# Kernel optimization log

Measured on AMD Instinct MI355X. Metric: run time of the kernel, lower is better.

## Reference

```python
import jax, jax.numpy as jnp
import numpy as np

N_NODES = 50000
N_EDGES = 500000
D_IN, D_HID = 128, 256


def _add_self_loops(edge_index, n):
    loop = jnp.arange(n, dtype=edge_index.dtype)
    src = jnp.concatenate([edge_index[0], loop])
    dst = jnp.concatenate([edge_index[1], loop])
    return src, dst


def _gcn_layer(x, W, b, src, dst, dinv_sqrt, n):
    # x: [N, d_in] -> h: [N, d_out]
    h = x @ W
    # symmetric normalization D^{-1/2} (A+I) D^{-1/2}
    norm = dinv_sqrt[src] * dinv_sqrt[dst]          # [E+N]
    msg = h[src] * norm[:, None]                    # gather + scale
    agg = jax.ops.segment_sum(msg, dst, num_segments=n)  # scatter-add
    return agg + b


def setup_inputs() -> dict:
    key = jax.random.key(0)
    ks = jax.random.split(key, 8)
    x = jax.random.normal(ks[0], (N_NODES, D_IN), dtype=jnp.float32)
    edge_index = jax.random.randint(ks[1], (2, N_EDGES), 0, N_NODES, dtype=jnp.int64 if jax.config.read('jax_enable_x64') else jnp.int32)
    s = lambda fan_in: 1.0 / np.sqrt(fan_in)
    W1 = jax.random.uniform(ks[2], (D_IN, D_HID), jnp.float32, -s(D_IN), s(D_IN))
    b1 = jnp.zeros((D_HID,), jnp.float32)
    W2 = jax.random.uniform(ks[3], (D_HID, D_HID), jnp.float32, -s(D_HID), s(D_HID))
    b2 = jnp.zeros((D_HID,), jnp.float32)
    W3 = jax.random.uniform(ks[4], (D_HID, D_HID), jnp.float32, -s(D_HID), s(D_HID))
    b3 = jnp.zeros((D_HID,), jnp.float32)
    return {"x": x, "edge_index": edge_index, "W1": W1, "b1": b1,
            "W2": W2, "b2": b2, "W3": W3, "b3": b3}


def reference(x, edge_index, W1, b1, W2, b2, W3, b3):
    n = x.shape[0]
    src, dst = _add_self_loops(edge_index, n)
    # degree includes self loops (edge weight 1), as in torch_geometric GCNConv
    deg = jax.ops.segment_sum(jnp.ones_like(dst, dtype=x.dtype), dst, num_segments=n)
    dinv_sqrt = jnp.where(deg > 0, jax.lax.rsqrt(jnp.maximum(deg, 1e-12)), 0.0)
    h = jax.nn.relu(_gcn_layer(x, W1, b1, src, dst, dinv_sqrt, n))
    h = jax.nn.relu(_gcn_layer(h, W2, b2, src, dst, dinv_sqrt, n))
    h = _gcn_layer(h, W3, b3, src, dst, dinv_sqrt, n)
    return h
```

## Files before the change

### kernel.cpp

```cpp
#include <hip/hip_runtime.h>

#define NNODES 50000
#define NEDGES 500000
#define DIN 128
#define DHID 256
#define MPAD 50048
#define NI4 12500
#define NSB 49

typedef unsigned short u16;
typedef __attribute__((ext_vector_type(8))) _Float16 half8;
typedef __attribute__((ext_vector_type(4))) float f32x4;

__device__ __forceinline__ u16 f2h(float f) {
  union { _Float16 h; u16 u; } v; v.h = (_Float16)f; return v.u;
}
__device__ __forceinline__ float h2f(unsigned int u) {
  union { _Float16 h; u16 u; } v; v.u = (u16)u; return (float)v.h;
}

#define GLDS16(g, l) __builtin_amdgcn_global_load_lds( \
    (const __attribute__((address_space(1))) void*)(g), \
    (__attribute__((address_space(3))) void*)(l), 16, 0, 0)

__global__ void k_zero_i32(int* __restrict__ p, int n) {
  int i = blockIdx.x * blockDim.x + threadIdx.x;
  if (i < n) p[i] = 0;
}

__global__ void k_hist(const int* __restrict__ dst, int* __restrict__ deg, int e) {
  int i = blockIdx.x * blockDim.x + threadIdx.x;
  if (i < e) atomicAdd(&deg[dst[i]], 1);
}

__global__ __launch_bounds__(256) void k_blocksum(const int* __restrict__ deg,
                                                  int* __restrict__ partials) {
  __shared__ int red[256];
  int tid = threadIdx.x;
  int t4 = blockIdx.x * 256 + tid;
  int sum = 0;
  if (t4 < NI4) {
    int4 v = ((const int4*)deg)[t4];
    sum = v.x + v.y + v.z + v.w;
  }
  red[tid] = sum;
  __syncthreads();
  for (int off = 128; off > 0; off >>= 1) {
    if (tid < off) red[tid] += red[tid + off];
    __syncthreads();
  }
  if (tid == 0) partials[blockIdx.x] = red[0];
}

__global__ __launch_bounds__(256) void k_scan2(int* __restrict__ deg,
                                               const int* __restrict__ partials,
                                               int* __restrict__ row_ptr,
                                               float* __restrict__ dinv) {
  __shared__ int sdata[256];
  __shared__ int sprefix;
  int tid = threadIdx.x, bid = blockIdx.x;
  int t4 = bid * 256 + tid;
  int4 v = make_int4(0, 0, 0, 0);
  if (t4 < NI4) v = ((const int4*)deg)[t4];
  int tsum = v.x + v.y + v.z + v.w;
  sdata[tid] = tsum;
  if (tid == 0) {
    int pre = 0;
    for (int b = 0; b < bid; ++b) pre += partials[b];
    sprefix = pre;
  }
  __syncthreads();
  for (int off = 1; off < 256; off <<= 1) {
    int val = (tid >= off) ? sdata[tid - off] : 0;
    __syncthreads();
    sdata[tid] += val;
    __syncthreads();
  }
  if (t4 < NI4) {
    int run = sdata[tid] - tsum + sprefix;
    int base = t4 * 4;
    float4 dv;
    dv.x = rsqrtf((float)v.x + 1.0f);
    dv.y = rsqrtf((float)v.y + 1.0f);
    dv.z = rsqrtf((float)v.z + 1.0f);
    dv.w = rsqrtf((float)v.w + 1.0f);
    *(float4*)(dinv + base) = dv;
    row_ptr[base + 0] = run; run += v.x;
    row_ptr[base + 1] = run; run += v.y;
    row_ptr[base + 2] = run; run += v.z;
    row_ptr[base + 3] = run; run += v.w;
    if (base + 4 == NNODES) row_ptr[NNODES] = run;
    ((int4*)deg)[t4] = make_int4(0, 0, 0, 0);
  }
}

__global__ void k_fill(const int* __restrict__ src, const int* __restrict__ dst,
                       const float* __restrict__ dinv, const int* __restrict__ row_ptr,
                       int* __restrict__ cursor, int* __restrict__ csr_src,
                       float* __restrict__ csr_nrm, int e) {
  int i = blockIdx.x * blockDim.x + threadIdx.x;
  if (i < e) {
    int d = dst[i], s = src[i];
    int pos = row_ptr[d] + atomicAdd(&cursor[d], 1);
    csr_src[pos] = s;
    csr_nrm[pos] = dinv[s] * dinv[d];
  }
}

__global__ void k_x2f16(const float* __restrict__ x, u16* __restrict__ xh, int total4) {
  int i = blockIdx.x * blockDim.x + threadIdx.x;
  if (i >= total4) return;
  float4 v = ((const float4*)x)[i];
  ushort4 o;
  o.x = f2h(v.x); o.y = f2h(v.y); o.z = f2h(v.z); o.w = f2h(v.w);
  ((ushort4*)xh)[i] = o;
}

__global__ void k_splitW3(const float* __restrict__ W1f, u16* __restrict__ P1,
                          const float* __restrict__ W2f, u16* __restrict__ P2,
                          const float* __restrict__ W3f, u16* __restrict__ P3) {
  int i = blockIdx.x * blockDim.x + threadIdx.x;
  const int s1 = DIN * 256, s2 = s1 + DHID * 256, s3 = s2 + DHID * 256;
  if (i >= s3) return;
  const float* W; u16* P; int li;
  if (i < s1)      { W = W1f; P = P1; li = i; }
  else if (i < s2) { W = W2f; P = P2; li = i - s1; }
  else             { W = W3f; P = P3; li = i - s2; }
  int k = li >> 8, n = li & 255;
  int t = k >> 5, q = (k >> 3) & 3, j = k & 7;
  int c = n >> 4, m = n & 15;
  int f = (c * 64 + q * 16 + m) * 8 + j;
  float w = W[li] * 256.0f;
  u16 hi = f2h(w);
  u16 lo = f2h(w - h2f(hi));
  P[(size_t)t * 16384 + f] = hi;
  P[(size_t)t * 16384 + 8192 + f] = lo;
}

template<int CPL>
__global__ __launch_bounds__(256) void k_aggF(const u16* __restrict__ hf,
                                              const float* __restrict__ dinv,
                                              const int* __restrict__ row_ptr,
                                              const int* __restrict__ csr_src,
                                              const float* __restrict__ csr_nrm,
                                              u16* __restrict__ aout, int n) {
  const int W = 64 * CPL;
  int node = blockIdx.x * 4 + (threadIdx.x >> 6);
  if (node >= n) return;
  int lane = threadIdx.x & 63;
  int c = lane * CPL;

  float acc[CPL];
  float di = dinv[node];
  float s2 = di * di;

  auto ldh = [&](int row, float* v) {
    const u16* p = hf + (size_t)row * W + c;
    if constexpr (CPL == 2) {
      unsigned int u = *(const unsigned int*)p;
      v[0] = h2f(u & 0xffffu); v[1] = h2f(u >> 16);
    } else {
      uint2 u = *(const uint2*)p;
      v[0] = h2f(u.x & 0xffffu); v[1] = h2f(u.x >> 16);
      v[2] = h2f(u.y & 0xffffu); v[3] = h2f(u.y >> 16);
    }
  };

  {
    float v[CPL];
    ldh(node, v);
#pragma unroll
    for (int j = 0; j < CPL; ++j) acc[j] = s2 * v[j];
  }

  int p = row_ptr[node], p1 = row_ptr[node + 1];
  for (; p + 4 <= p1; p += 4) {
    int s0 = csr_src[p], s1 = csr_src[p + 1], s2i = csr_src[p + 2], s3 = csr_src[p + 3];
    float w0 = csr_nrm[p], w1 = csr_nrm[p + 1], w2 = csr_nrm[p + 2], w3 = csr_nrm[p + 3];
    float v0[CPL], v1[CPL], v2[CPL], v3[CPL];
    ldh(s0, v0); ldh(s1, v1); ldh(s2i, v2); ldh(s3, v3);
#pragma unroll
    for (int j = 0; j < CPL; ++j) {
      acc[j] = fmaf(w0, v0[j], acc[j]);
      acc[j] = fmaf(w1, v1[j], acc[j]);
      acc[j] = fmaf(w2, v2[j], acc[j]);
      acc[j] = fmaf(w3, v3[j], acc[j]);
    }
  }
  for (; p < p1; ++p) {
    int s = csr_src[p];
    float w = csr_nrm[p];
    float v[CPL];
    ldh(s, v);
#pragma unroll
    for (int j = 0; j < CPL; ++j) acc[j] = fmaf(w, v[j], acc[j]);
  }

  if constexpr (CPL == 2) {
    ushort2 o;
    o.x = f2h(acc[0]); o.y = f2h(acc[1]);
    *(ushort2*)(aout + (size_t)node * W + c) = o;
  } else {
    ushort4 o;
    o.x = f2h(acc[0]); o.y = f2h(acc[1]); o.z = f2h(acc[2]); o.w = f2h(acc[3]);
    *(ushort4*)(aout + (size_t)node * W + c) = o;
  }
}

template<int K, int EPI>
__global__ __launch_bounds__(256, 4) void k_gemm_mfma(const u16* __restrict__ A,
                                                      const u16* __restrict__ Bpk,
                                                      const float* __restrict__ bias,
                                                      u16* __restrict__ hf16,
                                                      float* __restrict__ outf) {
  __shared__ __align__(16) u16 Bs[16384];
  const int lane = threadIdx.x & 63;
  const int wave = threadIdx.x >> 6;
  const int rw = wave & 1, cw = wave >> 1;
  const int m0 = blockIdx.x * 64 + rw * 32;

  f32x4 acc0[8], acc1[8];
#pragma unroll
  for (int c = 0; c < 8; ++c) {
    acc0[c] = {0.f, 0.f, 0.f, 0.f};
    acc1[c] = {0.f, 0.f, 0.f, 0.f};
  }

  const u16* a0p = A + (size_t)(m0 + (lane & 15)) * K + ((lane >> 4) * 8);
  const u16* a1p = a0p + (size_t)16 * K;

  for (int t = 0; t < K / 32; ++t) {
    __syncthreads();
    {
      const char* gsrc = (const char*)(Bpk + (size_t)t * 16384);
      char* lbase = (char*)Bs;
#pragma unroll
      for (int it = 0; it < 8; ++it) {
        int off = (wave * 8 + it) * 1024 + lane * 16;
        GLDS16(gsrc + off, lbase + off);
      }
    }
    __syncthreads();

    half8 a0 = *(const half8*)(a0p + t * 32);
    half8 a1 = *(const half8*)(a1p + t * 32);
#pragma unroll
    for (int c = 0; c < 8; ++c) {
      const u16* fb = Bs + ((cw * 8 + c) * 64 + lane) * 8;
      half8 bh = *(const half8*)fb;
      half8 bl = *(const half8*)(fb + 8192);
      acc0[c] = __builtin_amdgcn_mfma_f32_16x16x32_f16(a0, bh, acc0[c], 0, 0, 0);
      acc0[c] = __builtin_amdgcn_mfma_f32_16x16x32_f16(a0, bl, acc0[c], 0, 0, 0);
      acc1[c] = __builtin_amdgcn_mfma_f32_16x16x32_f16(a1, bh, acc1[c], 0, 0, 0);
      acc1[c] = __builtin_amdgcn_mfma_f32_16x16x32_f16(a1, bl, acc1[c], 0, 0, 0);
    }
  }

  const int cbase = lane & 15;
  const int r0 = m0 + ((lane >> 4) * 4);
  const float sc = 1.0f / 256.0f;
#pragma unroll
  for (int c = 0; c < 8; ++c) {
    int col = (cw * 8 + c) * 16 + cbase;
    float bv = bias[col];
#pragma unroll
    for (int r = 0; r < 4; ++r) {
      float v0 = fmaf(acc0[c][r], sc, bv);
      float v1 = fmaf(acc1[c][r], sc, bv);
      if (EPI == 0) {
        v0 = fmaxf(v0, 0.f);
        v1 = fmaxf(v1, 0.f);
        hf16[(size_t)(r0 + r) * 256 + col] = f2h(v0);
        hf16[(size_t)(r0 + 16 + r) * 256 + col] = f2h(v1);
      } else {
        if (r0 + r < NNODES) outf[(size_t)(r0 + r) * 256 + col] = v0;
        if (r0 + 16 + r < NNODES) outf[(size_t)(r0 + 16 + r) * 256 + col] = v1;
      }
    }
  }
}

extern "C" void kernel_launch(void* const* d_in, const int* in_sizes, int n_in,
                              void* d_out, int out_size, void* d_ws, size_t ws_size,
                              hipStream_t stream) {
  const float* x  = (const float*)d_in[0];
  const int*   ei = (const int*)d_in[1];
  const float* W1 = (const float*)d_in[2];
  const float* b1 = (const float*)d_in[3];
  const float* W2 = (const float*)d_in[4];
  const float* b2 = (const float*)d_in[5];
  const float* W3 = (const float*)d_in[6];
  const float* b3 = (const float*)d_in[7];
  float* out = (float*)d_out;
  (void)in_sizes; (void)n_in; (void)out_size; (void)ws_size;

  char* ws = (char*)d_ws;
  size_t off = 0;
  auto alloc = [&](size_t bytes) -> void* {
    void* p = (void*)(ws + off);
    off += (bytes + 255) & ~(size_t)255;
    return p;
  };
  float* dinv    = (float*)alloc((size_t)NNODES * 4);
  int*   deg     = (int*)alloc((size_t)NNODES * 4);
  int*   row_ptr = (int*)alloc((size_t)(NNODES + 1) * 4);
  int*   partials= (int*)alloc((size_t)NSB * 4);
  int*   csr_src = (int*)alloc((size_t)NEDGES * 4);
  float* csr_nrm = (float*)alloc((size_t)NEDGES * 4);
  u16*   xh      = (u16*)alloc((size_t)NNODES * DIN * 2);
  u16*   hbuf    = (u16*)alloc((size_t)MPAD * 256 * 2);
  u16*   A1      = (u16*)alloc((size_t)MPAD * DIN * 2);
  u16*   A2      = (u16*)alloc((size_t)MPAD * 256 * 2);
  u16*   W1pk    = (u16*)alloc((size_t)(DIN / 32) * 16384 * 2);
  u16*   W2pk    = (u16*)alloc((size_t)(DHID / 32) * 16384 * 2);
  u16*   W3pk    = (u16*)alloc((size_t)(DHID / 32) * 16384 * 2);

  const int* e_src = ei;
  const int* e_dst = ei + NEDGES;

  const int tb = 256;
  k_zero_i32<<<(NNODES + tb - 1) / tb, tb, 0, stream>>>(deg, NNODES);
  k_hist<<<(NEDGES + tb - 1) / tb, tb, 0, stream>>>(e_dst, deg, NEDGES);
  k_blocksum<<<NSB, 256, 0, stream>>>(deg, partials);
  k_scan2<<<NSB, 256, 0, stream>>>(deg, partials, row_ptr, dinv);
  k_fill<<<(NEDGES + tb - 1) / tb, tb, 0, stream>>>(e_src, e_dst, dinv, row_ptr, deg,
                                                    csr_src, csr_nrm, NEDGES);

  int x4 = NNODES * DIN / 4;
  k_x2f16<<<(x4 + tb - 1) / tb, tb, 0, stream>>>(x, xh, x4);
  int wtot = (DIN + DHID + DHID) * 256;
  k_splitW3<<<(wtot + tb - 1) / tb, tb, 0, stream>>>(W1, W1pk, W2, W2pk, W3, W3pk);

  const int gblocks = MPAD / 64;
  const int ablocks = (NNODES + 3) / 4;

  k_aggF<2><<<ablocks, 256, 0, stream>>>(xh, dinv, row_ptr, csr_src, csr_nrm,
                                         A1, NNODES);
  k_gemm_mfma<DIN, 0><<<gblocks, 256, 0, stream>>>(A1, W1pk, b1, hbuf, nullptr);
  k_aggF<4><<<ablocks, 256, 0, stream>>>(hbuf, dinv, row_ptr, csr_src, csr_nrm,
                                         A2, NNODES);
  k_gemm_mfma<DHID, 0><<<gblocks, 256, 0, stream>>>(A2, W2pk, b2, hbuf, nullptr);
  k_aggF<4><<<ablocks, 256, 0, stream>>>(hbuf, dinv, row_ptr, csr_src, csr_nrm,
                                         A2, NNODES);
  k_gemm_mfma<DHID, 1><<<gblocks, 256, 0, stream>>>(A2, W3pk, b3, nullptr, out);
}
```

Baseline: 345.8 us.

## Split wave across edges with 16-byte row loads and shuffle-reduce in aggregation

The aggregation kernel now gives each lane 8 fp16 features loaded with 16-byte vector loads. Lane groups in a wave process different neighbour edges at the same time, and the partial sums are combined with cross-lane shuffles. The kernel also becomes grid-stride over a fixed grid of 2048 blocks. The aim is more memory-level parallelism per wave and fewer, wider gather loads, at the cost of shuffle reductions and idle lanes on low-degree nodes.

Result: no change. 339.1 us (-1.9%).

```diff
diff --git a/kernel.cpp b/kernel.cpp
--- a/kernel.cpp
+++ b/kernel.cpp
@@ -137,73 +137,77 @@
   P[(size_t)t * 16384 + 8192 + f] = lo;
 }
 
-template<int CPL>
-__global__ __launch_bounds__(256) void k_aggF(const u16* __restrict__ hf,
+template<int W>
+__global__ __launch_bounds__(256) void k_aggG(const u16* __restrict__ hf,
                                               const float* __restrict__ dinv,
                                               const int* __restrict__ row_ptr,
                                               const int* __restrict__ csr_src,
                                               const float* __restrict__ csr_nrm,
                                               u16* __restrict__ aout, int n) {
-  const int W = 64 * CPL;
-  int node = blockIdx.x * 4 + (threadIdx.x >> 6);
-  if (node >= n) return;
-  int lane = threadIdx.x & 63;
-  int c = lane * CPL;
-
-  float acc[CPL];
-  float di = dinv[node];
-  float s2 = di * di;
-
-  auto ldh = [&](int row, float* v) {
-    const u16* p = hf + (size_t)row * W + c;
-    if constexpr (CPL == 2) {
-      unsigned int u = *(const unsigned int*)p;
-      v[0] = h2f(u & 0xffffu); v[1] = h2f(u >> 16);
-    } else {
-      uint2 u = *(const uint2*)p;
+  constexpr int GL = W / 8;
+  constexpr int NG = 64 / GL;
+  const int lane = threadIdx.x & 63;
+  const int wave = threadIdx.x >> 6;
+  const int g = lane / GL;
+  const int sub = lane % GL;
+  const int coff = sub * 8;
+
+  for (int node = blockIdx.x * 4 + wave; node < n; node += gridDim.x * 4) {
+    float acc[8];
+    float di = dinv[node];
+    float s2 = (g == 0) ? di * di : 0.0f;
+
+    auto ldrow = [&](int row, float* v) {
+      const uint4 u = *(const uint4*)(hf + (size_t)row * W + coff);
       v[0] = h2f(u.x & 0xffffu); v[1] = h2f(u.x >> 16);
       v[2] = h2f(u.y & 0xffffu); v[3] = h2f(u.y >> 16);
-    }
-  };
-
-  {
-    float v[CPL];
-    ldh(node, v);
-#pragma unroll
-    for (int j = 0; j < CPL; ++j) acc[j] = s2 * v[j];
-  }
-
-  int p = row_ptr[node], p1 = row_ptr[node + 1];
-  for (; p + 4 <= p1; p += 4) {
-    int s0 = csr_src[p], s1 = csr_src[p + 1], s2i = csr_src[p + 2], s3 = csr_src[p + 3];
-    float w0 = csr_nrm[p], w1 = csr_nrm[p + 1], w2 = csr_nrm[p + 2], w3 = csr_nrm[p + 3];
-    float v0[CPL], v1[CPL], v2[CPL], v3[CPL];
-    ldh(s0, v0); ldh(s1, v1); ldh(s2i, v2); ldh(s3, v3);
-#pragma unroll
-    for (int j = 0; j < CPL; ++j) {
-      acc[j] = fmaf(w0, v0[j], acc[j]);
-      acc[j] = fmaf(w1, v1[j], acc[j]);
-      acc[j] = fmaf(w2, v2[j], acc[j]);
-      acc[j] = fmaf(w3, v3[j], acc[j]);
-    }
-  }
-  for (; p < p1; ++p) {
-    int s = csr_src[p];
-    float w = csr_nrm[p];
-    float v[CPL];
-    ldh(s, v);
-#pragma unroll
-    for (int j = 0; j < CPL; ++j) acc[j] = fmaf(w, v[j], acc[j]);
-  }
-
-  if constexpr (CPL == 2) {
-    ushort2 o;
-    o.x = f2h(acc[0]); o.y = f2h(acc[1]);
-    *(ushort2*)(aout + (size_t)node * W + c) = o;
-  } else {
-    ushort4 o;
-    o.x = f2h(acc[0]); o.y = f2h(acc[1]); o.z = f2h(acc[2]); o.w = f2h(acc[3]);
-    *(ushort4*)(aout + (size_t)node * W + c) = o;
+      v[4] = h2f(u.z & 0xffffu); v[5] = h2f(u.z >> 16);
+      v[6] = h2f(u.w & 0xffffu); v[7] = h2f(u.w >> 16);
+    };
+
+    {
+      float v[8];
+      ldrow(node, v);
+#pragma unroll
+      for (int j = 0; j < 8; ++j) acc[j] = s2 * v[j];
+    }
+
+    const int p1 = row_ptr[node + 1];
+    int e = row_ptr[node] + g;
+    for (; e + NG < p1; e += 2 * NG) {
+      int s0 = csr_src[e], s1 = csr_src[e + NG];
+      float w0 = csr_nrm[e], w1 = csr_nrm[e + NG];
+      float v0[8], v1[8];
+      ldrow(s0, v0); ldrow(s1, v1);
+#pragma unroll
+      for (int j = 0; j < 8; ++j) {
+        acc[j] = fmaf(w0, v0[j], acc[j]);
+        acc[j] = fmaf(w1, v1[j], acc[j]);
+      }
+    }
+    if (e < p1) {
+      int s = csr_src[e];
+      float w = csr_nrm[e];
+      float v[8];
+      ldrow(s, v);
+#pragma unroll
+      for (int j = 0; j < 8; ++j) acc[j] = fmaf(w, v[j], acc[j]);
+    }
+
+#pragma unroll
+    for (int j = 0; j < 8; ++j) {
+      if constexpr (NG == 4) acc[j] += __shfl_xor(acc[j], 16);
+      acc[j] += __shfl_xor(acc[j], 32);
+    }
+
+    if (g == 0) {
+      uint4 o;
+      o.x = (unsigned)f2h(acc[0]) | ((unsigned)f2h(acc[1]) << 16);
+      o.y = (unsigned)f2h(acc[2]) | ((unsigned)f2h(acc[3]) << 16);
+      o.z = (unsigned)f2h(acc[4]) | ((unsigned)f2h(acc[5]) << 16);
+      o.w = (unsigned)f2h(acc[6]) | ((unsigned)f2h(acc[7]) << 16);
+      *(uint4*)(aout + (size_t)node * W + coff) = o;
+    }
   }
 }
 
@@ -332,15 +336,15 @@
   k_splitW3<<<(wtot + tb - 1) / tb, tb, 0, stream>>>(W1, W1pk, W2, W2pk, W3, W3pk);
 
   const int gblocks = MPAD / 64;
-  const int ablocks = (NNODES + 3) / 4;
-
-  k_aggF<2><<<ablocks, 256, 0, stream>>>(xh, dinv, row_ptr, csr_src, csr_nrm,
-                                         A1, NNODES);
+  const int aggrid = 2048;
+
+  k_aggG<128><<<aggrid, 256, 0, stream>>>(xh, dinv, row_ptr, csr_src, csr_nrm,
+                                          A1, NNODES);
   k_gemm_mfma<DIN, 0><<<gblocks, 256, 0, stream>>>(A1, W1pk, b1, hbuf, nullptr);
-  k_aggF<4><<<ablocks, 256, 0, stream>>>(hbuf, dinv, row_ptr, csr_src, csr_nrm,
-                                         A2, NNODES);
+  k_aggG<256><<<aggrid, 256, 0, stream>>>(hbuf, dinv, row_ptr, csr_src, csr_nrm,
+                                          A2, NNODES);
   k_gemm_mfma<DHID, 0><<<gblocks, 256, 0, stream>>>(A2, W2pk, b2, hbuf, nullptr);
-  k_aggF<4><<<ablocks, 256, 0, stream>>>(hbuf, dinv, row_ptr, csr_src, csr_nrm,
-                                         A2, NNODES);
+  k_aggG<256><<<aggrid, 256, 0, stream>>>(hbuf, dinv, row_ptr, csr_src, csr_nrm,
+                                          A2, NNODES);
   k_gemm_mfma<DHID, 1><<<gblocks, 256, 0, stream>>>(A2, W3pk, b3, nullptr, out);
 }
```
